# Performance work log

Measured on AMD Instinct MI355X. Metric: run time of the kernel, lower is better.

The kernel has to match this reference:

```python
import jax, jax.numpy as jnp
import numpy as np

K = 9
KS = (K - 1) // 2  # k_self
C_LIGHT = 299792458.0 / 1e6 / 600.0  # speed of light in detector units (as in HLayer)
BN_EPS = 1e-3  # keras BatchNormalization default epsilon


def _win2(f):
    # (B, N) -> (B, N, K): out[b, n, k] = f[b, n + k - KS], zero-padded at boundaries
    B, N = f.shape
    fp = jnp.pad(f, ((0, 0), (KS, KS)))
    return jnp.stack([fp[:, k:k + N] for k in range(K)], axis=2)


def _win3(f):
    # (B, N, F) -> (B, N, K, F): same shift-window along N
    B, N, F = f.shape
    fp = jnp.pad(f, ((0, 0), (KS, KS), (0, 0)))
    return jnp.stack([fp[:, k:k + N, :] for k in range(K)], axis=2)


def _valid_mask(N):
    # (N, K): True where neighbor index n + k - KS is in range
    idx = jnp.arange(N)[:, None] + jnp.arange(K)[None, :] - KS
    return (idx >= 0) & (idx < N)


def _hlayer(x):
    # x: (B, N, 6) with cols (t, c, a, px, py, pz) -> (B, N, K, 12)
    t, c, a = x[..., 0], x[..., 1], x[..., 2]
    px, py, pz = x[..., 3], x[..., 4], x[..., 5]
    N = x.shape[1]
    valid = _valid_mask(N)[None, :, :]  # (1, N, K)

    def d(f):  # shifted minus self, zeroed at boundaries (matches TF pad of the diff)
        return jnp.where(valid, _win2(f) - f[:, :, None], 0.0)

    dt, dx, dy, dz = d(t), d(px), d(py), d(pz)
    eu2 = dx * dx + dy * dy + dz * dz
    euclidean = jnp.sqrt(eu2)
    lorentz = (C_LIGHT * dt) ** 2 - eu2
    feats = [_win2(t), _win2(px), _win2(py), _win2(pz), _win2(c), _win2(a),
             dt, dx, dy, dz, euclidean, lorentz]
    return jnp.stack(feats, axis=3)  # (B, N, K, 12)


def _conv_bn(x, W, b, gamma, beta, mean, var):
    # kernel-size-1 Conv1D with relu activation, then inference-mode BatchNorm
    y = jax.nn.relu(jnp.matmul(x, W) + b)
    return gamma * (y - mean) * jax.lax.rsqrt(var + BN_EPS) + beta


def _make_params(key, dims):
    params = {}
    for i, (fi, fo) in enumerate(zip(dims[:-1], dims[1:])):
        key, k1 = jax.random.split(key)
        s = np.sqrt(2.0 / fi)
        params[f'W{i}'] = jax.random.normal(k1, (fi, fo), jnp.float32) * s
        params[f'b{i}'] = jnp.zeros((fo,), jnp.float32)
        key, k2, k3, k4 = jax.random.split(key, 4)
        params[f'g{i}'] = 1.0 + 0.1 * jax.random.normal(k2, (fo,), jnp.float32)
        params[f'be{i}'] = 0.1 * jax.random.normal(k3, (fo,), jnp.float32)
        params[f'mu{i}'] = 0.1 * jax.random.normal(k4, (fo,), jnp.float32)
        params[f'var{i}'] = 0.5 + jax.random.uniform(key, (fo,), jnp.float32)
    return params


def setup_inputs() -> dict:
    key = jax.random.key(0)
    kx, km, kf = jax.random.split(key, 3)
    B, N = 8, 4096
    x = jax.random.normal(kx, (B, N, 6), jnp.float32)
    dims_m = [12, 128, 256]   # MLayer/CRLayer stack on H features
    dims_f = [6, 128, 256]    # FRLayer stack on raw inputs
    pm = _make_params(km, dims_m)
    pf = _make_params(kf, dims_f)
    inp = {'x': x}
    for i in range(2):
        for n in ['W', 'b', 'g', 'be', 'mu', 'var']:
            inp[f'm_{n}{i}'] = pm[f'{n}{i}']
            inp[f'f_{n}{i}'] = pf[f'{n}{i}']
    return inp


def reference(x,
              m_W0, m_b0, m_g0, m_be0, m_mu0, m_var0,
              m_W1, m_b1, m_g1, m_be1, m_mu1, m_var1,
              f_W0, f_b0, f_g0, f_be0, f_mu0, f_var0,
              f_W1, f_b1, f_g1, f_be1, f_mu1, f_var1):
    # H-layer: (B, N, 6) -> (B, N, K, 12) geometric neighbor features
    h = _hlayer(x)
    # M branch (CRLayer, 1x1 convs over feature dim): -> m_nkf (B, N, K, 256)
    m = _conv_bn(h, m_W0, m_b0, m_g0, m_be0, m_mu0, m_var0)
    m = _conv_bn(m, m_W1, m_b1, m_g1, m_be1, m_mu1, m_var1)
    # FR branch on raw inputs: -> fr_nf (B, N, 256)
    fr = _conv_bn(x, f_W0, f_b0, f_g0, f_be0, f_mu0, f_var0)
    fr = _conv_bn(fr, f_W1, f_b1, f_g1, f_be1, f_mu1, f_var1)
    # A-layer: gate shifted fr by m and max-aggregate over K neighbors
    fr_sh = _win3(fr)                      # (B, N, K, 256), zero-padded shifts
    T = m * fr_sh                          # (B, N, K, 256)
    return jnp.max(T, axis=2)              # (B, N, 256)
```

## Files before the change

kernel.cpp:

```cpp
#include <hip/hip_runtime.h>

#define N_PTS 4096
#define C_LIGHT 0.49965409666666664f
#define BN_EPS 1e-3f

typedef __attribute__((ext_vector_type(8))) short short8;
typedef __attribute__((ext_vector_type(4))) float f32x4;

static __device__ __forceinline__ unsigned short f2bf(float f) {
    unsigned u = __float_as_uint(f);
    u += 0x7FFFu + ((u >> 16) & 1u);
    return (unsigned short)(u >> 16);
}
static __device__ __forceinline__ float bf2f(unsigned short h) {
    return __uint_as_float(((unsigned)h) << 16);
}

__global__ __launch_bounds__(256) void fold_kernel(
    const float* __restrict__ mW1, const float* __restrict__ mb1,
    const float* __restrict__ mg0, const float* __restrict__ mbe0,
    const float* __restrict__ mmu0, const float* __restrict__ mvar0,
    const float* __restrict__ mg1, const float* __restrict__ mbe1,
    const float* __restrict__ mmu1, const float* __restrict__ mvar1,
    const float* __restrict__ fW1p, const float* __restrict__ fb1,
    const float* __restrict__ fg0, const float* __restrict__ fbe0,
    const float* __restrict__ fmu0, const float* __restrict__ fvar0,
    const float* __restrict__ fg1, const float* __restrict__ fbe1,
    const float* __restrict__ fmu1, const float* __restrict__ fvar1,
    float* __restrict__ mBf, float* __restrict__ mS1, float* __restrict__ mT1,
    unsigned short* __restrict__ mWhi, unsigned short* __restrict__ mWlo,
    float* __restrict__ fBf, float* __restrict__ fS1, float* __restrict__ fT1,
    unsigned short* __restrict__ fWhi, unsigned short* __restrict__ fWlo)
{
    int br = blockIdx.x;
    const float* W1  = br ? fW1p : mW1;
    const float* b1  = br ? fb1  : mb1;
    const float* g0  = br ? fg0  : mg0;
    const float* be0 = br ? fbe0 : mbe0;
    const float* mu0 = br ? fmu0 : mmu0;
    const float* var0= br ? fvar0: mvar0;
    const float* g1  = br ? fg1  : mg1;
    const float* be1 = br ? fbe1 : mbe1;
    const float* mu1 = br ? fmu1 : mmu1;
    const float* var1= br ? fvar1: mvar1;
    float* Bf = br ? fBf : mBf;
    float* S1 = br ? fS1 : mS1;
    float* T1 = br ? fT1 : mT1;
    unsigned short* Whi = br ? fWhi : mWhi;
    unsigned short* Wlo = br ? fWlo : mWlo;

    __shared__ float s0s[128], t0s[128];
    int t = threadIdx.x;
    if (t < 128) {
        float s = g0[t] / sqrtf(var0[t] + BN_EPS);
        s0s[t] = s;
        t0s[t] = be0[t] - mu0[t] * s;
    }
    __syncthreads();

    {
        float s1 = g1[t] / sqrtf(var1[t] + BN_EPS);
        S1[t] = s1;
        T1[t] = be1[t] - mu1[t] * s1;
        float acc = b1[t];
        for (int i = 0; i < 128; ++i) acc = fmaf(t0s[i], W1[i * 256 + t], acc);
        Bf[t] = acc;
    }

    for (int e = t; e < 32768; e += 256) {
        int j = e & 7, l = (e >> 3) & 63, ks = (e >> 9) & 3, ct = e >> 11;
        int i = ks * 32 + (l >> 4) * 8 + j;
        int c = ct * 16 + (l & 15);
        float w = s0s[i] * W1[i * 256 + c];
        unsigned short hi = f2bf(w);
        unsigned short lo = f2bf(w - bf2f(hi));
        Whi[e] = hi;
        Wlo[e] = lo;
    }
}

__global__ __launch_bounds__(256, 2) void fr_kernel(
    const float* __restrict__ x,
    const float* __restrict__ W0,
    const float* __restrict__ b0,
    const short8* __restrict__ WfHi, const short8* __restrict__ WfLo,
    const float* __restrict__ Bf, const float* __restrict__ S1,
    const float* __restrict__ T1,
    float* __restrict__ fr)
{
    __shared__ float xs[64][6];
    __shared__ __attribute__((aligned(16))) float w0s[6][136];
    __shared__ __attribute__((aligned(16))) float b0s[128];
    __shared__ __attribute__((aligned(16))) unsigned short hAhi[4 * 64 * 8];
    __shared__ __attribute__((aligned(16))) unsigned short hAlo[4 * 64 * 8];

    int t = threadIdx.x;
    long row0 = (long)blockIdx.x * 64;

    for (int i = t; i < 384; i += 256) xs[i / 6][i % 6] = x[row0 * 6 + i];
    for (int i = t; i < 768; i += 256) w0s[i >> 7][i & 127] = W0[i];
    if (t < 128) b0s[t] = b0[t];

    int lane = t & 63, wv = t >> 6;
    int laneN = lane & 15, laneH = lane >> 4;
    int cg = t & 7;

    float bfv[4], s1v[4], t1v[4];
    int colc[4];
#pragma unroll
    for (int c = 0; c < 4; ++c) {
        colc[c] = (wv * 4 + c) * 16 + laneN;
        bfv[c] = Bf[colc[c]];
        s1v[c] = S1[colc[c]];
        t1v[c] = T1[colc[c]];
    }
    f32x4 acc[4][4];
#pragma unroll
    for (int mt = 0; mt < 4; ++mt)
#pragma unroll
        for (int c = 0; c < 4; ++c) {
            f32x4 z = {bfv[c], bfv[c], bfv[c], bfv[c]};
            acc[mt][c] = z;
        }
    __syncthreads();

    for (int ks = 0; ks < 4; ++ks) {
        int k0 = ks * 32 + cg * 4;
        float4 wreg[6];
#pragma unroll
        for (int i = 0; i < 6; ++i) wreg[i] = *(const float4*)&w0s[i][k0];
        float4 bq = *(const float4*)&b0s[k0];

        for (int idx = t; idx < 512; idx += 256) {
            int row = idx >> 3;
            float a0 = bq.x, a1 = bq.y, a2 = bq.z, a3 = bq.w;
#pragma unroll
            for (int i = 0; i < 6; ++i) {
                float hv = xs[row][i];
                a0 = fmaf(hv, wreg[i].x, a0);
                a1 = fmaf(hv, wreg[i].y, a1);
                a2 = fmaf(hv, wreg[i].z, a2);
                a3 = fmaf(hv, wreg[i].w, a3);
            }
            a0 = fmaxf(a0, 0.f); a1 = fmaxf(a1, 0.f);
            a2 = fmaxf(a2, 0.f); a3 = fmaxf(a3, 0.f);
            unsigned short h0 = f2bf(a0), h1 = f2bf(a1), h2 = f2bf(a2), h3 = f2bf(a3);
            unsigned short l0 = f2bf(a0 - bf2f(h0)), l1 = f2bf(a1 - bf2f(h1));
            unsigned short l2 = f2bf(a2 - bf2f(h2)), l3 = f2bf(a3 - bf2f(h3));
            int mt = row >> 4, nl = row & 15;
            int base = (mt * 64 + (cg >> 1) * 16 + nl) * 8 + (cg & 1) * 4;
            uint2 hv2; hv2.x = (unsigned)h0 | ((unsigned)h1 << 16);
            hv2.y = (unsigned)h2 | ((unsigned)h3 << 16);
            *(uint2*)&hAhi[base] = hv2;
            uint2 lv2; lv2.x = (unsigned)l0 | ((unsigned)l1 << 16);
            lv2.y = (unsigned)l2 | ((unsigned)l3 << 16);
            *(uint2*)&hAlo[base] = lv2;
        }
        __syncthreads();

        short8 Bhi[4], Blo[4];
#pragma unroll
        for (int c = 0; c < 4; ++c) {
            int fo = ((wv * 4 + c) * 4 + ks) * 64 + lane;
            Bhi[c] = WfHi[fo];
            Blo[c] = WfLo[fo];
        }
#pragma unroll
        for (int mt = 0; mt < 4; ++mt) {
            short8 Ahi = *(const short8*)&hAhi[(mt * 64 + lane) * 8];
            short8 Alo = *(const short8*)&hAlo[(mt * 64 + lane) * 8];
#pragma unroll
            for (int c = 0; c < 4; ++c) {
                f32x4 a = acc[mt][c];
                a = __builtin_amdgcn_mfma_f32_16x16x32_bf16(Alo, Bhi[c], a, 0, 0, 0);
                a = __builtin_amdgcn_mfma_f32_16x16x32_bf16(Ahi, Blo[c], a, 0, 0, 0);
                a = __builtin_amdgcn_mfma_f32_16x16x32_bf16(Ahi, Bhi[c], a, 0, 0, 0);
                acc[mt][c] = a;
            }
        }
        __syncthreads();
    }

#pragma unroll
    for (int c = 0; c < 4; ++c)
#pragma unroll
        for (int mt = 0; mt < 4; ++mt)
#pragma unroll
            for (int r = 0; r < 4; ++r) {
                float y = fmaf(fmaxf(acc[mt][c][r], 0.f), s1v[c], t1v[c]);
                fr[(row0 + mt * 16 + laneH * 4 + r) * 256 + colc[c]] = y;
            }
}

__global__ __launch_bounds__(256, 2) void fused_kernel(
    const float* __restrict__ x,
    const float* __restrict__ W0,
    const float* __restrict__ b0,
    const short8* __restrict__ WfHi, const short8* __restrict__ WfLo,
    const float* __restrict__ Bf, const float* __restrict__ S1,
    const float* __restrict__ T1,
    const float* __restrict__ fr,
    float* __restrict__ out)
{
    __shared__ float xs[24][6];
    __shared__ float hf_s[144][12];
    __shared__ __attribute__((aligned(16))) float w0s[12][136];
    __shared__ __attribute__((aligned(16))) float b0s[128];
    __shared__ __attribute__((aligned(16))) unsigned short hAhi[9 * 64 * 8];
    __shared__ __attribute__((aligned(16))) unsigned short hAlo[9 * 64 * 8];

    int t = threadIdx.x;
    int bn = blockIdx.x;
    int b  = bn >> 8;
    int n0 = (bn & 255) << 4;
    const float* xb = x + (long)b * N_PTS * 6;

    if (t < 144) {
        int rr = t / 6, cc = t % 6;
        int n = n0 - 4 + rr;
        xs[rr][cc] = (n >= 0 && n < N_PTS) ? xb[n * 6 + cc] : 0.f;
    }
    for (int i = t; i < 12 * 128; i += 256) w0s[i >> 7][i & 127] = W0[i];
    if (t < 128) b0s[t] = b0[t];
    __syncthreads();

    if (t < 144) {
        int kt = t >> 4, nl = t & 15;
        const float* self = xs[nl + 4];
        const float* nb   = xs[nl + kt];
        int nbn = n0 + nl + kt - 4;
        float msk = (nbn >= 0 && nbn < N_PTS) ? 1.f : 0.f;
        float dt = (nb[0] - self[0]) * msk;
        float dx = (nb[3] - self[3]) * msk;
        float dy = (nb[4] - self[4]) * msk;
        float dz = (nb[5] - self[5]) * msk;
        float eu2 = dx * dx + dy * dy + dz * dz;
        hf_s[t][0]  = nb[0];
        hf_s[t][1]  = nb[3];
        hf_s[t][2]  = nb[4];
        hf_s[t][3]  = nb[5];
        hf_s[t][4]  = nb[1];
        hf_s[t][5]  = nb[2];
        hf_s[t][6]  = dt;
        hf_s[t][7]  = dx;
        hf_s[t][8]  = dy;
        hf_s[t][9]  = dz;
        hf_s[t][10] = sqrtf(eu2);
        float cdt = C_LIGHT * dt;
        hf_s[t][11] = cdt * cdt - eu2;
    }

    int lane = t & 63, wv = t >> 6;
    int laneN = lane & 15, laneH = lane >> 4;
    int cg = t & 7;

    float bfv[4], s1v[4], t1v[4];
    int colc[4];
#pragma unroll
    for (int c = 0; c < 4; ++c) {
        colc[c] = (wv * 4 + c) * 16 + laneN;
        bfv[c] = Bf[colc[c]];
        s1v[c] = S1[colc[c]];
        t1v[c] = T1[colc[c]];
    }
    f32x4 acc[9][4];
#pragma unroll
    for (int kt = 0; kt < 9; ++kt)
#pragma unroll
        for (int c = 0; c < 4; ++c) {
            f32x4 z = {bfv[c], bfv[c], bfv[c], bfv[c]};
            acc[kt][c] = z;
        }
    __syncthreads();

    for (int ks = 0; ks < 4; ++ks) {
        int k0 = ks * 32 + cg * 4;
        float4 wreg[12];
#pragma unroll
        for (int i = 0; i < 12; ++i) wreg[i] = *(const float4*)&w0s[i][k0];
        float4 bq = *(const float4*)&b0s[k0];

        for (int idx = t; idx < 1152; idx += 256) {
            int row = idx >> 3;
            float a0 = bq.x, a1 = bq.y, a2 = bq.z, a3 = bq.w;
#pragma unroll
            for (int i = 0; i < 12; ++i) {
                float hv = hf_s[row][i];
                a0 = fmaf(hv, wreg[i].x, a0);
                a1 = fmaf(hv, wreg[i].y, a1);
                a2 = fmaf(hv, wreg[i].z, a2);
                a3 = fmaf(hv, wreg[i].w, a3);
            }
            a0 = fmaxf(a0, 0.f); a1 = fmaxf(a1, 0.f);
            a2 = fmaxf(a2, 0.f); a3 = fmaxf(a3, 0.f);
            unsigned short h0 = f2bf(a0), h1 = f2bf(a1), h2 = f2bf(a2), h3 = f2bf(a3);
            unsigned short l0 = f2bf(a0 - bf2f(h0)), l1 = f2bf(a1 - bf2f(h1));
            unsigned short l2 = f2bf(a2 - bf2f(h2)), l3 = f2bf(a3 - bf2f(h3));
            int kt = row >> 4, nl = row & 15;
            int base = (kt * 64 + (cg >> 1) * 16 + nl) * 8 + (cg & 1) * 4;
            uint2 hv2; hv2.x = (unsigned)h0 | ((unsigned)h1 << 16);
            hv2.y = (unsigned)h2 | ((unsigned)h3 << 16);
            *(uint2*)&hAhi[base] = hv2;
            uint2 lv2; lv2.x = (unsigned)l0 | ((unsigned)l1 << 16);
            lv2.y = (unsigned)l2 | ((unsigned)l3 << 16);
            *(uint2*)&hAlo[base] = lv2;
        }
        __syncthreads();

        short8 Bhi[4], Blo[4];
#pragma unroll
        for (int c = 0; c < 4; ++c) {
            int fo = ((wv * 4 + c) * 4 + ks) * 64 + lane;
            Bhi[c] = WfHi[fo];
            Blo[c] = WfLo[fo];
        }
#pragma unroll
        for (int kt = 0; kt < 9; ++kt) {
            short8 Ahi = *(const short8*)&hAhi[(kt * 64 + lane) * 8];
            short8 Alo = *(const short8*)&hAlo[(kt * 64 + lane) * 8];
#pragma unroll
            for (int c = 0; c < 4; ++c) {
                f32x4 a = acc[kt][c];
                a = __builtin_amdgcn_mfma_f32_16x16x32_bf16(Alo, Bhi[c], a, 0, 0, 0);
                a = __builtin_amdgcn_mfma_f32_16x16x32_bf16(Ahi, Blo[c], a, 0, 0, 0);
                a = __builtin_amdgcn_mfma_f32_16x16x32_bf16(Ahi, Bhi[c], a, 0, 0, 0);
                acc[kt][c] = a;
            }
        }
        __syncthreads();
    }

    const float* frb = fr + ((long)b << 20);
    float* outb = out + ((long)b << 20);
#pragma unroll
    for (int c = 0; c < 4; ++c) {
        float best[4];
#pragma unroll
        for (int kt = 0; kt < 9; ++kt) {
#pragma unroll
            for (int r = 0; r < 4; ++r) {
                int nl = laneH * 4 + r;
                int nbn = n0 + nl + kt - 4;
                float f = 0.f;
                if (nbn >= 0 && nbn < N_PTS) f = frb[nbn * 256 + colc[c]];
                float m = fmaf(fmaxf(acc[kt][c][r], 0.f), s1v[c], t1v[c]);
                float T = m * f;
                best[r] = (kt == 0) ? T : fmaxf(best[r], T);
            }
        }
#pragma unroll
        for (int r = 0; r < 4; ++r)
            outb[(n0 + laneH * 4 + r) * 256 + colc[c]] = best[r];
    }
}

extern "C" void kernel_launch(void* const* d_in, const int* in_sizes, int n_in,
                              void* d_out, int out_size, void* d_ws, size_t ws_size,
                              hipStream_t stream)
{
    const float* x = (const float*)d_in[0];
    const float* m_W0  = (const float*)d_in[1];
    const float* f_W0  = (const float*)d_in[2];
    const float* m_b0  = (const float*)d_in[3];
    const float* f_b0  = (const float*)d_in[4];
    const float* m_g0  = (const float*)d_in[5];
    const float* f_g0  = (const float*)d_in[6];
    const float* m_be0 = (const float*)d_in[7];
    const float* f_be0 = (const float*)d_in[8];
    const float* m_mu0 = (const float*)d_in[9];
    const float* f_mu0 = (const float*)d_in[10];
    const float* m_var0= (const float*)d_in[11];
    const float* f_var0= (const float*)d_in[12];
    const float* m_W1  = (const float*)d_in[13];
    const float* f_W1  = (const float*)d_in[14];
    const float* m_b1  = (const float*)d_in[15];
    const float* f_b1  = (const float*)d_in[16];
    const float* m_g1  = (const float*)d_in[17];
    const float* f_g1  = (const float*)d_in[18];
    const float* m_be1 = (const float*)d_in[19];
    const float* f_be1 = (const float*)d_in[20];
    const float* m_mu1 = (const float*)d_in[21];
    const float* f_mu1 = (const float*)d_in[22];
    const float* m_var1= (const float*)d_in[23];
    const float* f_var1= (const float*)d_in[24];

    char* wsb = (char*)d_ws;
    float* fr  = (float*)wsb;
    float* mBf = (float*)(wsb + 33554432);
    float* mS1 = mBf + 256;
    float* mT1 = mS1 + 256;
    float* fBf = mT1 + 256;
    float* fS1 = fBf + 256;
    float* fT1 = fS1 + 256;
    unsigned short* mWhi = (unsigned short*)(fT1 + 256);
    unsigned short* mWlo = mWhi + 32768;
    unsigned short* fWhi = mWlo + 32768;
    unsigned short* fWlo = fWhi + 32768;

    fold_kernel<<<2, 256, 0, stream>>>(
        m_W1, m_b1, m_g0, m_be0, m_mu0, m_var0, m_g1, m_be1, m_mu1, m_var1,
        f_W1, f_b1, f_g0, f_be0, f_mu0, f_var0, f_g1, f_be1, f_mu1, f_var1,
        mBf, mS1, mT1, mWhi, mWlo,
        fBf, fS1, fT1, fWhi, fWlo);

    fr_kernel<<<8 * N_PTS / 64, 256, 0, stream>>>(
        x, f_W0, f_b0, (const short8*)fWhi, (const short8*)fWlo,
        fBf, fS1, fT1, fr);

    fused_kernel<<<8 * N_PTS / 16, 256, 0, stream>>>(
        x, m_W0, m_b0, (const short8*)mWhi, (const short8*)mWlo,
        mBf, mS1, mT1, fr, (float*)d_out);
}
```

Baseline: 234.9 us.

## Store fr transposed, stage neighbor window and output tile through LDS

fr_kernel now writes fr channel-major (frT) with float4 stores. fused_kernel loads a 32-point halo window per channel from frT into shared memory, reusing it across the 9 neighbors instead of issuing 36 scattered global loads per channel group. It also stages output in LDS for coalesced float4 stores. BF16 hi/lo splitting uses packed conversion intrinsics, and shared memory is unioned into one buffer so the new staging areas cost little extra LDS, which could still affect occupancy.

```diff
diff --git a/kernel.cpp b/kernel.cpp
--- a/kernel.cpp
+++ b/kernel.cpp
@@ -1,4 +1,5 @@
 #include <hip/hip_runtime.h>
+#include <hip/hip_bf16.h>
 
 #define N_PTS 4096
 #define C_LIGHT 0.49965409666666664f
@@ -14,6 +15,12 @@
 }
 static __device__ __forceinline__ float bf2f(unsigned short h) {
     return __uint_as_float(((unsigned)h) << 16);
+}
+static __device__ __forceinline__ unsigned pk2(float a, float b) {
+    __hip_bfloat162 h = __float22bfloat162_rn(make_float2(a, b));
+    union { __hip_bfloat162 v; unsigned u; } cv;
+    cv.v = h;
+    return cv.u;
 }
 
 __global__ __launch_bounds__(256) void fold_kernel(
@@ -86,7 +93,7 @@
     const short8* __restrict__ WfHi, const short8* __restrict__ WfLo,
     const float* __restrict__ Bf, const float* __restrict__ S1,
     const float* __restrict__ T1,
-    float* __restrict__ fr)
+    float* __restrict__ frT)
 {
     __shared__ float xs[64][6];
     __shared__ __attribute__((aligned(16))) float w0s[6][136];
@@ -144,17 +151,16 @@
             }
             a0 = fmaxf(a0, 0.f); a1 = fmaxf(a1, 0.f);
             a2 = fmaxf(a2, 0.f); a3 = fmaxf(a3, 0.f);
-            unsigned short h0 = f2bf(a0), h1 = f2bf(a1), h2 = f2bf(a2), h3 = f2bf(a3);
-            unsigned short l0 = f2bf(a0 - bf2f(h0)), l1 = f2bf(a1 - bf2f(h1));
-            unsigned short l2 = f2bf(a2 - bf2f(h2)), l3 = f2bf(a3 - bf2f(h3));
+            unsigned hi01 = pk2(a0, a1), hi23 = pk2(a2, a3);
+            float q0 = __uint_as_float(hi01 << 16);
+            float q1 = __uint_as_float(hi01 & 0xffff0000u);
+            float q2 = __uint_as_float(hi23 << 16);
+            float q3 = __uint_as_float(hi23 & 0xffff0000u);
+            unsigned lo01 = pk2(a0 - q0, a1 - q1), lo23 = pk2(a2 - q2, a3 - q3);
             int mt = row >> 4, nl = row & 15;
             int base = (mt * 64 + (cg >> 1) * 16 + nl) * 8 + (cg & 1) * 4;
-            uint2 hv2; hv2.x = (unsigned)h0 | ((unsigned)h1 << 16);
-            hv2.y = (unsigned)h2 | ((unsigned)h3 << 16);
-            *(uint2*)&hAhi[base] = hv2;
-            uint2 lv2; lv2.x = (unsigned)l0 | ((unsigned)l1 << 16);
-            lv2.y = (unsigned)l2 | ((unsigned)l3 << 16);
-            *(uint2*)&hAlo[base] = lv2;
+            *(uint2*)&hAhi[base] = make_uint2(hi01, hi23);
+            *(uint2*)&hAlo[base] = make_uint2(lo01, lo23);
         }
         __syncthreads();
 
@@ -184,13 +190,25 @@
 #pragma unroll
     for (int c = 0; c < 4; ++c)
 #pragma unroll
-        for (int mt = 0; mt < 4; ++mt)
-#pragma unroll
-            for (int r = 0; r < 4; ++r) {
-                float y = fmaf(fmaxf(acc[mt][c][r], 0.f), s1v[c], t1v[c]);
-                fr[(row0 + mt * 16 + laneH * 4 + r) * 256 + colc[c]] = y;
-            }
-}
+        for (int mt = 0; mt < 4; ++mt) {
+            float4 o;
+            o.x = fmaf(fmaxf(acc[mt][c][0], 0.f), s1v[c], t1v[c]);
+            o.y = fmaf(fmaxf(acc[mt][c][1], 0.f), s1v[c], t1v[c]);
+            o.z = fmaf(fmaxf(acc[mt][c][2], 0.f), s1v[c], t1v[c]);
+            o.w = fmaf(fmaxf(acc[mt][c][3], 0.f), s1v[c], t1v[c]);
+            *(float4*)&frT[(long)colc[c] * 32768 + row0 + mt * 16 + laneH * 4] = o;
+        }
+}
+
+#define SM_XS   0
+#define SM_B0   576
+#define SM_W0   1088
+#define SM_HF   7616
+#define SM_AHI  14528
+#define SM_ALO  23744
+#define SM_FRT  0
+#define SM_OUT  33792
+#define SM_TOT  50432
 
 __global__ __launch_bounds__(256, 2) void fused_kernel(
     const float* __restrict__ x,
@@ -199,15 +217,18 @@
     const short8* __restrict__ WfHi, const short8* __restrict__ WfLo,
     const float* __restrict__ Bf, const float* __restrict__ S1,
     const float* __restrict__ T1,
-    const float* __restrict__ fr,
+    const float* __restrict__ frT,
     float* __restrict__ out)
 {
-    __shared__ float xs[24][6];
-    __shared__ float hf_s[144][12];
-    __shared__ __attribute__((aligned(16))) float w0s[12][136];
-    __shared__ __attribute__((aligned(16))) float b0s[128];
-    __shared__ __attribute__((aligned(16))) unsigned short hAhi[9 * 64 * 8];
-    __shared__ __attribute__((aligned(16))) unsigned short hAlo[9 * 64 * 8];
+    __shared__ __attribute__((aligned(16))) char smem[SM_TOT];
+    float* xs  = (float*)(smem + SM_XS);
+    float* b0s = (float*)(smem + SM_B0);
+    float* w0s = (float*)(smem + SM_W0);
+    float* hfp = (float*)(smem + SM_HF);
+    unsigned short* hAhi = (unsigned short*)(smem + SM_AHI);
+    unsigned short* hAlo = (unsigned short*)(smem + SM_ALO);
+    float* frL = (float*)(smem + SM_FRT);
+    float* oL  = (float*)(smem + SM_OUT);
 
     int t = threadIdx.x;
     int bn = blockIdx.x;
@@ -218,16 +239,16 @@
     if (t < 144) {
         int rr = t / 6, cc = t % 6;
         int n = n0 - 4 + rr;
-        xs[rr][cc] = (n >= 0 && n < N_PTS) ? xb[n * 6 + cc] : 0.f;
-    }
-    for (int i = t; i < 12 * 128; i += 256) w0s[i >> 7][i & 127] = W0[i];
+        xs[rr * 6 + cc] = (n >= 0 && n < N_PTS) ? xb[n * 6 + cc] : 0.f;
+    }
+    for (int i = t; i < 12 * 128; i += 256) w0s[(i >> 7) * 136 + (i & 127)] = W0[i];
     if (t < 128) b0s[t] = b0[t];
     __syncthreads();
 
     if (t < 144) {
         int kt = t >> 4, nl = t & 15;
-        const float* self = xs[nl + 4];
-        const float* nb   = xs[nl + kt];
+        const float* self = &xs[(nl + 4) * 6];
+        const float* nb   = &xs[(nl + kt) * 6];
         int nbn = n0 + nl + kt - 4;
         float msk = (nbn >= 0 && nbn < N_PTS) ? 1.f : 0.f;
         float dt = (nb[0] - self[0]) * msk;
@@ -235,19 +256,20 @@
         float dy = (nb[4] - self[4]) * msk;
         float dz = (nb[5] - self[5]) * msk;
         float eu2 = dx * dx + dy * dy + dz * dz;
-        hf_s[t][0]  = nb[0];
-        hf_s[t][1]  = nb[3];
-        hf_s[t][2]  = nb[4];
-        hf_s[t][3]  = nb[5];
-        hf_s[t][4]  = nb[1];
-        hf_s[t][5]  = nb[2];
-        hf_s[t][6]  = dt;
-        hf_s[t][7]  = dx;
-        hf_s[t][8]  = dy;
-        hf_s[t][9]  = dz;
-        hf_s[t][10] = sqrtf(eu2);
+        float* h = &hfp[t * 12];
+        h[0]  = nb[0];
+        h[1]  = nb[3];
+        h[2]  = nb[4];
+        h[3]  = nb[5];
+        h[4]  = nb[1];
+        h[5]  = nb[2];
+        h[6]  = dt;
+        h[7]  = dx;
+        h[8]  = dy;
+        h[9]  = dz;
+        h[10] = sqrtf(eu2);
         float cdt = C_LIGHT * dt;
-        hf_s[t][11] = cdt * cdt - eu2;
+        h[11] = cdt * cdt - eu2;
     }
 
     int lane = t & 63, wv = t >> 6;
@@ -277,7 +299,7 @@
         int k0 = ks * 32 + cg * 4;
         float4 wreg[12];
 #pragma unroll
-        for (int i = 0; i < 12; ++i) wreg[i] = *(const float4*)&w0s[i][k0];
+        for (int i = 0; i < 12; ++i) wreg[i] = *(const float4*)&w0s[i * 136 + k0];
         float4 bq = *(const float4*)&b0s[k0];
 
         for (int idx = t; idx < 1152; idx += 256) {
@@ -285,7 +307,7 @@
             float a0 = bq.x, a1 = bq.y, a2 = bq.z, a3 = bq.w;
 #pragma unroll
             for (int i = 0; i < 12; ++i) {
-                float hv = hf_s[row][i];
+                float hv = hfp[row * 12 + i];
                 a0 = fmaf(hv, wreg[i].x, a0);
                 a1 = fmaf(hv, wreg[i].y, a1);
                 a2 = fmaf(hv, wreg[i].z, a2);
@@ -293,17 +315,16 @@
             }
             a0 = fmaxf(a0, 0.f); a1 = fmaxf(a1, 0.f);
             a2 = fmaxf(a2, 0.f); a3 = fmaxf(a3, 0.f);
-            unsigned short h0 = f2bf(a0), h1 = f2bf(a1), h2 = f2bf(a2), h3 = f2bf(a3);
-            unsigned short l0 = f2bf(a0 - bf2f(h0)), l1 = f2bf(a1 - bf2f(h1));
-            unsigned short l2 = f2bf(a2 - bf2f(h2)), l3 = f2bf(a3 - bf2f(h3));
+            unsigned hi01 = pk2(a0, a1), hi23 = pk2(a2, a3);
+            float q0 = __uint_as_float(hi01 << 16);
+            float q1 = __uint_as_float(hi01 & 0xffff0000u);
+            float q2 = __uint_as_float(hi23 << 16);
+            float q3 = __uint_as_float(hi23 & 0xffff0000u);
+            unsigned lo01 = pk2(a0 - q0, a1 - q1), lo23 = pk2(a2 - q2, a3 - q3);
             int kt = row >> 4, nl = row & 15;
             int base = (kt * 64 + (cg >> 1) * 16 + nl) * 8 + (cg & 1) * 4;
-            uint2 hv2; hv2.x = (unsigned)h0 | ((unsigned)h1 << 16);
-            hv2.y = (unsigned)h2 | ((unsigned)h3 << 16);
-            *(uint2*)&hAhi[base] = hv2;
-            uint2 lv2; lv2.x = (unsigned)l0 | ((unsigned)l1 << 16);
-            lv2.y = (unsigned)l2 | ((unsigned)l3 << 16);
-            *(uint2*)&hAlo[base] = lv2;
+            *(uint2*)&hAhi[base] = make_uint2(hi01, hi23);
+            *(uint2*)&hAlo[base] = make_uint2(lo01, lo23);
         }
         __syncthreads();
 
@@ -329,28 +350,41 @@
         }
         __syncthreads();
     }
-
-    const float* frb = fr + ((long)b << 20);
+    for (int i = t; i < 2048; i += 256) {
+        int col = i >> 3, seg = i & 7;
+        int nn = n0 - 8 + seg * 4;
+        float4 v = make_float4(0.f, 0.f, 0.f, 0.f);
+        if (nn >= 0 && nn < N_PTS)
+            v = *(const float4*)&frT[(long)col * 32768 + (b << 12) + nn];
+        *(float4*)&frL[col * 33 + seg * 4] = v;
+    }
+    __syncthreads();
+
+#pragma unroll
+    for (int c = 0; c < 4; ++c) {
+        float fv[12];
+        int fb = colc[c] * 33 + laneH * 4 + 4;
+#pragma unroll
+        for (int j = 0; j < 12; ++j) fv[j] = frL[fb + j];
+#pragma unroll
+        for (int r = 0; r < 4; ++r) {
+            float best;
+#pragma unroll
+            for (int kt = 0; kt < 9; ++kt) {
+                float m = fmaf(fmaxf(acc[kt][c][r], 0.f), s1v[c], t1v[c]);
+                float T = m * fv[r + kt];
+                best = (kt == 0) ? T : fmaxf(best, T);
+            }
+            oL[(laneH * 4 + r) * 260 + colc[c]] = best;
+        }
+    }
+    __syncthreads();
+
     float* outb = out + ((long)b << 20);
-#pragma unroll
-    for (int c = 0; c < 4; ++c) {
-        float best[4];
-#pragma unroll
-        for (int kt = 0; kt < 9; ++kt) {
-#pragma unroll
-            for (int r = 0; r < 4; ++r) {
-                int nl = laneH * 4 + r;
-                int nbn = n0 + nl + kt - 4;
-                float f = 0.f;
-                if (nbn >= 0 && nbn < N_PTS) f = frb[nbn * 256 + colc[c]];
-                float m = fmaf(fmaxf(acc[kt][c][r], 0.f), s1v[c], t1v[c]);
-                float T = m * f;
-                best[r] = (kt == 0) ? T : fmaxf(best[r], T);
-            }
-        }
-#pragma unroll
-        for (int r = 0; r < 4; ++r)
-            outb[(n0 + laneH * 4 + r) * 256 + colc[c]] = best[r];
+    for (int i = t; i < 1024; i += 256) {
+        int row = i >> 6, c4 = (i & 63) << 2;
+        float4 v = *(const float4*)&oL[row * 260 + c4];
+        *(float4*)&outb[((long)(n0 + row) << 8) + c4] = v;
     }
 }
 
@@ -385,7 +419,7 @@
     const float* f_var1= (const float*)d_in[24];
 
     char* wsb = (char*)d_ws;
-    float* fr  = (float*)wsb;
+    float* frT = (float*)wsb;
     float* mBf = (float*)(wsb + 33554432);
     float* mS1 = mBf + 256;
     float* mT1 = mS1 + 256;
@@ -405,9 +439,9 @@
 
     fr_kernel<<<8 * N_PTS / 64, 256, 0, stream>>>(
         x, f_W0, f_b0, (const short8*)fWhi, (const short8*)fWlo,
-        fBf, fS1, fT1, fr);
+        fBf, fS1, fT1, frT);
 
     fused_kernel<<<8 * N_PTS / 16, 256, 0, stream>>>(
         x, m_W0, m_b0, (const short8*)mWhi, (const short8*)mWlo,
-        mBf, mS1, mT1, fr, (float*)d_out);
-}
+        mBf, mS1, mT1, frT, (float*)d_out);
+}
```

New measurement: 239.6 us. 2.0% more time.
